# Performance work log

Measured on AMD Instinct MI355X. Metric: run time of the kernel, lower is better.

Reference implementation:

```python
import jax, jax.numpy as jnp
import numpy as np

N = 100000
E = 800000
D_IN = 64
D_HID = 64
D_OUT = 47


def gcn_conv(x, edge_index, W, b):
    # GCNConv with normalize=False: linear transform then sum-aggregate over edges.
    h = x @ W                              # [N, d_out]
    src, dst = edge_index[0], edge_index[1]
    msg = h[src]                           # [E, d_out] gather
    agg = jax.ops.segment_sum(msg, dst, num_segments=N)  # [N, d_out] scatter-add
    return agg + b


def setup_inputs() -> dict:
    key = jax.random.key(0)
    ks = jax.random.split(key, 8)
    x = jax.random.normal(ks[0], (N, D_IN), dtype=jnp.float32)
    edge_index = jax.random.randint(ks[1], (2, E), 0, N, dtype=jnp.int64)
    # Glorot-ish init for weights, zeros for bias (as in GCNConv.reset_parameters)
    def glorot(k, fan_in, fan_out):
        s = jnp.sqrt(6.0 / (fan_in + fan_out))
        return jax.random.uniform(k, (fan_in, fan_out), jnp.float32, -s, s)
    W1 = glorot(ks[2], D_IN, D_HID)
    b1 = jnp.zeros((D_HID,), jnp.float32)
    W2 = glorot(ks[3], D_HID, D_HID)
    b2 = jnp.zeros((D_HID,), jnp.float32)
    W3 = glorot(ks[4], D_HID, D_OUT)
    b3 = jnp.zeros((D_OUT,), jnp.float32)
    return {"x": x, "edge_index": edge_index,
            "W1": W1, "b1": b1, "W2": W2, "b2": b2, "W3": W3, "b3": b3}


def reference(x, edge_index, W1, b1, W2, b2, W3, b3):
    # Layer 1: conv -> relu (dropout is identity at inference)
    h = jax.nn.relu(gcn_conv(x, edge_index, W1, b1))
    # Layer 2
    h = jax.nn.relu(gcn_conv(h, edge_index, W2, b2))
    # Output layer + log_softmax over classes
    out = gcn_conv(h, edge_index, W3, b3)
    return jax.nn.log_softmax(out, axis=-1)
```

## Files before the change

kernel.cpp:

```cpp
#include <hip/hip_runtime.h>
#include <cmath>


#define B1_EPB 4096
#define BKT_SH 8
#define CHUNK  256
#define PSTRIDE 512

typedef __attribute__((ext_vector_type(8))) short bf8;
typedef __attribute__((ext_vector_type(4))) float f4;

__device__ __forceinline__ unsigned int f2bf(float x) {
  unsigned int u = __float_as_uint(x);
  return (u + 0x7FFFu + ((u >> 16) & 1u)) >> 16;
}
__device__ __forceinline__ float bflo(unsigned int u) { return __uint_as_float(u << 16); }
__device__ __forceinline__ float bfhi(unsigned int u) { return __uint_as_float(u & 0xFFFF0000u); }

__global__ void bhist_cvt_k(const int* __restrict__ dsti, int* __restrict__ part,
                            int ne, const float* __restrict__ x,
                            unsigned short* __restrict__ xb, int n4,
                            int nbkt, int nseg) {
  __shared__ int lh[PSTRIDE];
  const int b = blockIdx.x, t = threadIdx.x;
  if (b < nseg) {
    for (int i = t; i < PSTRIDE; i += 256) lh[i] = 0;
    __syncthreads();
    const int base = b * B1_EPB;
    const int m = min(B1_EPB, ne - base);
    for (int i = t; i < m; i += 256) atomicAdd(&lh[dsti[base + i] >> BKT_SH], 1);
    __syncthreads();
    for (int i = t; i < PSTRIDE; i += 256) part[b * PSTRIDE + i] = lh[i];
  }
  const int gid = b * 256 + t, gst = gridDim.x * 256;
  for (int j = gid; j < n4; j += gst) {
    float4 v = ((const float4*)x)[j];
    ushort4 o;
    o.x = (unsigned short)f2bf(v.x); o.y = (unsigned short)f2bf(v.y);
    o.z = (unsigned short)f2bf(v.z); o.w = (unsigned short)f2bf(v.w);
    ((ushort4*)xb)[j] = o;
  }
}

__global__ void btot_k(const int* __restrict__ part, int* __restrict__ btot,
                       int nseg) {
  __shared__ int sh[256];
  const int t = threadIdx.x;
  const int bkt = (blockIdx.x << 6) + (t & 63);
  int s0 = 0, s1 = 0, s2 = 0, s3 = 0, s4 = 0, s5 = 0, s6 = 0, s7 = 0;
  int seg = t >> 6;
  for (; seg + 28 < nseg; seg += 32) {
    s0 += part[(seg +  0) * PSTRIDE + bkt];
    s1 += part[(seg +  4) * PSTRIDE + bkt];
    s2 += part[(seg +  8) * PSTRIDE + bkt];
    s3 += part[(seg + 12) * PSTRIDE + bkt];
    s4 += part[(seg + 16) * PSTRIDE + bkt];
    s5 += part[(seg + 20) * PSTRIDE + bkt];
    s6 += part[(seg + 24) * PSTRIDE + bkt];
    s7 += part[(seg + 28) * PSTRIDE + bkt];
  }
  for (; seg < nseg; seg += 4) s0 += part[seg * PSTRIDE + bkt];
  sh[t] = ((s0 + s1) + (s2 + s3)) + ((s4 + s5) + (s6 + s7));
  __syncthreads();
  if (t < 64) btot[bkt] = sh[t] + sh[t + 64] + sh[t + 128] + sh[t + 192];
}

__global__ void bscan_k(const int* __restrict__ btot, int* __restrict__ bbase,
                        int* __restrict__ bcur, int nbkt, int ne) {
  __shared__ int sh[512];
  const int t = threadIdx.x;
  const int s = btot[t];
  sh[t] = s; __syncthreads();
  for (int o = 1; o < 512; o <<= 1) {
    int v = (t >= o) ? sh[t - o] : 0; __syncthreads();
    sh[t] += v; __syncthreads();
  }
  if (t < nbkt) { int e = sh[t] - s; bbase[t] = e; bcur[t] = e; }
  if (t == 0) bbase[nbkt] = ne;
}

__global__ void bucket_k(const int* __restrict__ srci, const int* __restrict__ dsti,
                         const int* __restrict__ part, int* __restrict__ bcur,
                         uint2* __restrict__ ebuf, int ne, int nbkt) {
  __shared__ int lcur[512], lbase[512];
  const int t = threadIdx.x;
  const int base = blockIdx.x * B1_EPB;
  const int m = min(B1_EPB, ne - base);
  for (int i = t; i < nbkt; i += 256) {
    const int c = part[blockIdx.x * PSTRIDE + i];
    lbase[i] = c ? atomicAdd(&bcur[i], c) : 0;
    lcur[i] = 0;
  }
  __syncthreads();
  for (int i = t; i < m; i += 256) {
    const int s = srci[base + i], d = dsti[base + i];
    const int b = d >> BKT_SH;
    const int p = lbase[b] + atomicAdd(&lcur[b], 1);
    ebuf[p] = make_uint2((unsigned)s, (unsigned)d);
  }
}

__global__ void fillb_k(const uint2* __restrict__ ebuf, const int* __restrict__ bbase,
                        int* __restrict__ row_off, int* __restrict__ ssrc,
                        int n, int ne) {
  __shared__ int lcnt[256], lpre[256], lcur[256];
  const int b = blockIdx.x, t = threadIdx.x;
  const int v0 = b << BKT_SH;
  const int nv = min(1 << BKT_SH, n - v0);
  const int start = bbase[b], end = bbase[b + 1];
  lcnt[t] = 0; __syncthreads();
  for (int i = start + t; i < end; i += 256)
    atomicAdd(&lcnt[ebuf[i].y & ((1 << BKT_SH) - 1)], 1);
  __syncthreads();
  const int x = lcnt[t];
  lpre[t] = x; __syncthreads();
  for (int o = 1; o < 256; o <<= 1) {
    int v = (t >= o) ? lpre[t - o] : 0; __syncthreads();
    lpre[t] += v; __syncthreads();
  }
  const int excl = start + lpre[t] - x;
  lcur[t] = excl;
  if (t < nv) row_off[v0 + t] = excl;
  if (t == 0) row_off[v0 + nv] = end;
  __syncthreads();
  for (int i = start + t; i < end; i += 256) {
    const uint2 e = ebuf[i];
    const int p = atomicAdd(&lcur[e.y & ((1 << BKT_SH) - 1)], 1);
    ssrc[p] = (int)e.x;
  }
}

template <int DOUT, bool LS>
__launch_bounds__(256, 4)
__global__ void fused_k(const unsigned short* __restrict__ in,
                        const int* __restrict__ row_off, const int* __restrict__ ssrc,
                        const float* __restrict__ Wm, const float* __restrict__ bin,
                        void* __restrict__ outp, int n) {
  constexpr int NT = (DOUT + 15) / 16;
  const int lane  = threadIdx.x & 63;
  const int wslot = threadIdx.x >> 6;
  const int quad  = lane >> 4;
  const int f16i  = lane & 15;

  __shared__ char rows_raw[4][16 * 144];
  __shared__ int  sidx[4][CHUNK];
  __shared__ unsigned short Wt[64 * 72];
  char* my  = rows_raw[wslot];
  int*  sid = sidx[wslot];

  {
    const int t = threadIdx.x;
    for (int i = t; i < 64 * 72; i += 256) Wt[i] = 0;
    __syncthreads();
    for (int i = t; i < 64 * DOUT; i += 256) {
      const int k = i / DOUT, c = i - k * DOUT;
      Wt[c * 72 + k] = (unsigned short)f2bf(Wm[i]);
    }
  }
  float bc[NT];
#pragma unroll
  for (int t = 0; t < NT; ++t) {
    const int c = t * 16 + f16i;
    bc[t] = (c < DOUT) ? bin[c] : 0.f;
  }
  __syncthreads();

  const uint2* in2 = (const uint2*)in;
  const int wid = (int)((blockIdx.x * blockDim.x + threadIdx.x) >> 6);
  const int nwv = (int)((gridDim.x * blockDim.x) >> 6);
  const int ntiles = (n + 15) >> 4;

  for (int tile = wid; tile < ntiles; tile += nwv) {
    const int v0 = tile << 4;
    const int ro_l = row_off[min(v0 + min(lane, 16), n)];
    const int base     = __shfl(ro_l, 0, 64);
    const int tile_end = __shfl(ro_l, 16, 64);
    int ns[4], nE[4];
#pragma unroll
    for (int r = 0; r < 4; ++r) {
      const int m = quad * 4 + r;
      ns[r] = __shfl(ro_l, m, 64);
      nE[r] = __shfl(ro_l, m + 1, 64);
    }

    float4 accA[4], accB[4];
#pragma unroll
    for (int r = 0; r < 4; ++r) {
      accA[r] = make_float4(0.f, 0.f, 0.f, 0.f);
      accB[r] = make_float4(0.f, 0.f, 0.f, 0.f);
    }

    for (int off = base; off < tile_end; off += CHUNK) {
      const int cend = min(tile_end, off + CHUNK);
      const int nL = cend - off;
#pragma unroll
      for (int k = 0; k < CHUNK / 64; ++k) {
        const int p = off + lane + k * 64;
        if (p < cend) sid[lane + k * 64] = ssrc[p];
      }
      asm volatile("s_waitcnt lgkmcnt(0)" ::: "memory");

#pragma unroll
      for (int r = 0; r < 4; ++r) {
        const int ls = max(ns[r], off), le = min(nE[r], cend);
        for (int c = ls; c < le; c += 8) {
          uint2 q[8];
#pragma unroll
          for (int k = 0; k < 8; ++k) {
            const int lofs = min(c - off + k, nL - 1);
            const int s = sid[lofs];
            q[k] = (c + k < le) ? in2[(size_t)s * 16 + f16i]
                                : make_uint2(0u, 0u);
          }
#pragma unroll
          for (int k = 0; k < 8; k += 2) {
            accA[r].x += bflo(q[k].x); accB[r].x += bflo(q[k + 1].x);
            accA[r].y += bfhi(q[k].x); accB[r].y += bfhi(q[k + 1].x);
            accA[r].z += bflo(q[k].y); accB[r].z += bflo(q[k + 1].y);
            accA[r].w += bfhi(q[k].y); accB[r].w += bfhi(q[k + 1].y);
          }
        }
      }
    }

#pragma unroll
    for (int r = 0; r < 4; ++r) {
      const int m = quad * 4 + r;
      uint2 p;
      p.x = f2bf(accA[r].x + accB[r].x) | (f2bf(accA[r].y + accB[r].y) << 16);
      p.y = f2bf(accA[r].z + accB[r].z) | (f2bf(accA[r].w + accB[r].w) << 16);
      *(uint2*)(my + m * 144 + f16i * 8) = p;
    }
    asm volatile("s_waitcnt lgkmcnt(0)" ::: "memory");

    bf8 a0 = *(const bf8*)(my + f16i * 144 + quad * 16);
    bf8 a1 = *(const bf8*)(my + f16i * 144 + quad * 16 + 64);
    f4 acc[NT];
#pragma unroll
    for (int t = 0; t < NT; ++t) {
      const unsigned short* wp = Wt + (t * 16 + f16i) * 72 + quad * 8;
      bf8 w0 = *(const bf8*)(wp);
      bf8 w1 = *(const bf8*)(wp + 32);
      f4 z = {0.f, 0.f, 0.f, 0.f};
      acc[t] = __builtin_amdgcn_mfma_f32_16x16x32_bf16(a0, w0, z, 0, 0, 0);
      acc[t] = __builtin_amdgcn_mfma_f32_16x16x32_bf16(a1, w1, acc[t], 0, 0, 0);
    }

    if (!LS) {
      unsigned short* ob = (unsigned short*)outp;
#pragma unroll
      for (int t = 0; t < NT; ++t)
#pragma unroll
        for (int j = 0; j < 4; ++j) {
          const int v = v0 + quad * 4 + j;
          if (v < n) {
            float val = acc[t][j] + bc[t];
            ob[(size_t)v * 64 + t * 16 + f16i] =
                (unsigned short)f2bf(fmaxf(val, 0.f));
          }
        }
    } else {
      float* ob = (float*)outp;
      float val[NT][4];
#pragma unroll
      for (int t = 0; t < NT; ++t)
#pragma unroll
        for (int j = 0; j < 4; ++j) val[t][j] = acc[t][j] + bc[t];
#pragma unroll
      for (int j = 0; j < 4; ++j) {
        float mx = -INFINITY;
#pragma unroll
        for (int t = 0; t < NT; ++t)
          if (t * 16 + f16i < DOUT) mx = fmaxf(mx, val[t][j]);
#pragma unroll
        for (int o = 1; o <= 8; o <<= 1) mx = fmaxf(mx, __shfl_xor(mx, o, 64));
        float sm = 0.f;
#pragma unroll
        for (int t = 0; t < NT; ++t)
          if (t * 16 + f16i < DOUT) sm += __expf(val[t][j] - mx);
#pragma unroll
        for (int o = 1; o <= 8; o <<= 1) sm += __shfl_xor(sm, o, 64);
        const float lse = mx + __logf(sm);
        const int v = v0 + quad * 4 + j;
        if (v < n) {
#pragma unroll
          for (int t = 0; t < NT; ++t) {
            const int c = t * 16 + f16i;
            if (c < DOUT) ob[(size_t)v * DOUT + c] = val[t][j] - lse;
          }
        }
      }
    }
  }
}

extern "C" void kernel_launch(void* const* d_in, const int* in_sizes, int n_in,
                              void* d_out, int out_size, void* d_ws, size_t ws_size,
                              hipStream_t stream) {
  const float* x  = (const float*)d_in[0];
  const int*   ei = (const int*)d_in[1];
  const float* W1 = (const float*)d_in[2];
  const float* b1 = (const float*)d_in[3];
  const float* W2 = (const float*)d_in[4];
  const float* b2 = (const float*)d_in[5];
  const float* W3 = (const float*)d_in[6];
  const float* b3 = (const float*)d_in[7];
  float* outp = (float*)d_out;

  const int n  = in_sizes[0] / 64;
  const int ne = in_sizes[1] / 2;
  const int* srci = ei;
  const int* dsti = ei + ne;
  const int nbkt = (n + (1 << BKT_SH) - 1) >> BKT_SH;
  const int nseg = (ne + B1_EPB - 1) / B1_EPB;

  const size_t N64 = (size_t)n * 64;
  unsigned short* xb   = (unsigned short*)d_ws;
  unsigned short* bufA = xb + N64;
  unsigned short* bufB = bufA + N64;
  uint2* ebuf   = (uint2*)(bufB + N64);
  int* row_off  = (int*)(ebuf + ne);
  int* part     = row_off + n + 1;
  int* bbase    = part + nseg * PSTRIDE;
  int* bcur     = bbase + nbkt + 1;
  int* btot     = bcur + nbkt;
  int* ssrc     = btot + 512;

  const int TB = 256;
  const int fus_blocks = 1568;

  bhist_cvt_k<<<784, TB, 0, stream>>>(dsti, part, ne, x, xb, (int)(N64 / 4), nbkt, nseg);
  btot_k<<<8, TB, 0, stream>>>(part, btot, nseg);
  bscan_k<<<1, 512, 0, stream>>>(btot, bbase, bcur, nbkt, ne);
  bucket_k<<<nseg, TB, 0, stream>>>(srci, dsti, part, bcur, ebuf, ne, nbkt);
  fillb_k<<<nbkt, TB, 0, stream>>>(ebuf, bbase, row_off, ssrc, n, ne);

  fused_k<64, false><<<fus_blocks, TB, 0, stream>>>(xb,   row_off, ssrc, W1, b1, bufA, n);
  fused_k<64, false><<<fus_blocks, TB, 0, stream>>>(bufA, row_off, ssrc, W2, b2, bufB, n);
  fused_k<47, true ><<<fus_blocks, TB, 0, stream>>>(bufB, row_off, ssrc, W3, b3, outp, n);
}
```

Before: 208.3 us.

## Fuse three GCN layer kernels into one persistent kernel with grid barriers

Replaces the three per-layer kernel launches with a single persistent kernel of 1024 blocks that runs all three layers, separated by a software grid barrier built on an atomic counter and spin-wait. Tiles are handed out through an atomic work-stealing counter per layer instead of a static grid-stride loop, which evens out load across waves on the skewed-degree graph. The goal is to cut launch gaps and tail imbalance. The barrier assumes all 1024 blocks are resident at once (four per CU at this register and LDS budget) and has a guard timeout that could silently break ordering if that assumption fails.

```diff
diff --git a/kernel.cpp b/kernel.cpp
--- a/kernel.cpp
+++ b/kernel.cpp
@@ -6,6 +6,7 @@
 #define BKT_SH 8
 #define CHUNK  256
 #define PSTRIDE 512
+#define FUS_BLOCKS 1024
 
 typedef __attribute__((ext_vector_type(8))) short bf8;
 typedef __attribute__((ext_vector_type(4))) float f4;
@@ -66,7 +67,9 @@
 }
 
 __global__ void bscan_k(const int* __restrict__ btot, int* __restrict__ bbase,
-                        int* __restrict__ bcur, int nbkt, int ne) {
+                        int* __restrict__ bcur, int nbkt, int ne,
+                        int* __restrict__ bar, int* __restrict__ steal,
+                        int nwaves) {
   __shared__ int sh[512];
   const int t = threadIdx.x;
   const int s = btot[t];
@@ -76,7 +79,11 @@
     sh[t] += v; __syncthreads();
   }
   if (t < nbkt) { int e = sh[t] - s; bbase[t] = e; bcur[t] = e; }
-  if (t == 0) bbase[nbkt] = ne;
+  if (t == 0) {
+    bbase[nbkt] = ne;
+    bar[0] = 0;
+    steal[0] = nwaves; steal[1] = nwaves; steal[2] = nwaves;
+  }
 }
 
 __global__ void bucket_k(const int* __restrict__ srci, const int* __restrict__ dsti,
@@ -130,32 +137,39 @@
   }
 }
 
+__device__ __forceinline__ void gridbar(int* bar, int target) {
+  __syncthreads();
+  if (threadIdx.x == 0) {
+    __hip_atomic_fetch_add(bar, 1, __ATOMIC_ACQ_REL, __HIP_MEMORY_SCOPE_AGENT);
+    int guard = 0;
+    while (__hip_atomic_load(bar, __ATOMIC_ACQUIRE, __HIP_MEMORY_SCOPE_AGENT) < target &&
+           guard < (1 << 22)) {
+      __builtin_amdgcn_s_sleep(8);
+      ++guard;
+    }
+  }
+  __syncthreads();
+}
+
 template <int DOUT, bool LS>
-__launch_bounds__(256, 4)
-__global__ void fused_k(const unsigned short* __restrict__ in,
-                        const int* __restrict__ row_off, const int* __restrict__ ssrc,
-                        const float* __restrict__ Wm, const float* __restrict__ bin,
-                        void* __restrict__ outp, int n) {
+__device__ __forceinline__ void layer_pass(
+    const unsigned short* __restrict__ in, const int* __restrict__ row_off,
+    const int* __restrict__ ssrc, const float* __restrict__ Wm,
+    const float* __restrict__ bin, void* __restrict__ outp, int n,
+    unsigned short* Wt, char* my, int* sid, int* steal, int wid) {
   constexpr int NT = (DOUT + 15) / 16;
-  const int lane  = threadIdx.x & 63;
-  const int wslot = threadIdx.x >> 6;
-  const int quad  = lane >> 4;
-  const int f16i  = lane & 15;
-
-  __shared__ char rows_raw[4][16 * 144];
-  __shared__ int  sidx[4][CHUNK];
-  __shared__ unsigned short Wt[64 * 72];
-  char* my  = rows_raw[wslot];
-  int*  sid = sidx[wslot];
-
-  {
-    const int t = threadIdx.x;
-    for (int i = t; i < 64 * 72; i += 256) Wt[i] = 0;
+  const int tid  = threadIdx.x;
+  const int lane = tid & 63;
+  const int quad = lane >> 4;
+  const int f16i = lane & 15;
+
+  if (DOUT < 64) {
+    for (int i = tid; i < 64 * 72; i += 256) Wt[i] = 0;
     __syncthreads();
-    for (int i = t; i < 64 * DOUT; i += 256) {
-      const int k = i / DOUT, c = i - k * DOUT;
-      Wt[c * 72 + k] = (unsigned short)f2bf(Wm[i]);
-    }
+  }
+  for (int i = tid; i < 64 * DOUT; i += 256) {
+    const int k = i / DOUT, c = i - k * DOUT;
+    Wt[c * 72 + k] = (unsigned short)f2bf(Wm[i]);
   }
   float bc[NT];
 #pragma unroll
@@ -166,11 +180,10 @@
   __syncthreads();
 
   const uint2* in2 = (const uint2*)in;
-  const int wid = (int)((blockIdx.x * blockDim.x + threadIdx.x) >> 6);
-  const int nwv = (int)((gridDim.x * blockDim.x) >> 6);
   const int ntiles = (n + 15) >> 4;
 
-  for (int tile = wid; tile < ntiles; tile += nwv) {
+  int tile = wid;
+  while (tile < ntiles) {
     const int v0 = tile << 4;
     const int ro_l = row_off[min(v0 + min(lane, 16), n)];
     const int base     = __shfl(ro_l, 0, 64);
@@ -291,7 +304,37 @@
         }
       }
     }
-  }
+
+    int nt_ = 0;
+    if (lane == 0) nt_ = atomicAdd(steal, 1);
+    tile = __shfl(nt_, 0, 64);
+  }
+}
+
+__launch_bounds__(256, 4)
+__global__ void fused3_k(const unsigned short* __restrict__ xb,
+                         unsigned short* __restrict__ bufA,
+                         unsigned short* __restrict__ bufB,
+                         float* __restrict__ outp,
+                         const int* __restrict__ row_off,
+                         const int* __restrict__ ssrc,
+                         const float* __restrict__ W1, const float* __restrict__ b1,
+                         const float* __restrict__ W2, const float* __restrict__ b2,
+                         const float* __restrict__ W3, const float* __restrict__ b3,
+                         int n, int* __restrict__ bar, int* __restrict__ steal) {
+  __shared__ char rows_raw[4][16 * 144];
+  __shared__ int  sidx[4][CHUNK];
+  __shared__ unsigned short Wt[64 * 72];
+  const int wslot = threadIdx.x >> 6;
+  char* my  = rows_raw[wslot];
+  int*  sid = sidx[wslot];
+  const int wid = (int)((blockIdx.x * 256 + threadIdx.x) >> 6);
+
+  layer_pass<64, false>(xb,   row_off, ssrc, W1, b1, bufA, n, Wt, my, sid, steal + 0, wid);
+  gridbar(bar, (int)gridDim.x);
+  layer_pass<64, false>(bufA, row_off, ssrc, W2, b2, bufB, n, Wt, my, sid, steal + 1, wid);
+  gridbar(bar, 2 * (int)gridDim.x);
+  layer_pass<47, true >(bufB, row_off, ssrc, W3, b3, outp, n, Wt, my, sid, steal + 2, wid);
 }
 
 extern "C" void kernel_launch(void* const* d_in, const int* in_sizes, int n_in,
@@ -324,18 +367,19 @@
   int* bbase    = part + nseg * PSTRIDE;
   int* bcur     = bbase + nbkt + 1;
   int* btot     = bcur + nbkt;
-  int* ssrc     = btot + 512;
+  int* bar      = btot + 512;
+  int* steal    = bar + 1;
+  int* ssrc     = steal + 3;
 
   const int TB = 256;
-  const int fus_blocks = 1568;
+  const int nwaves = FUS_BLOCKS * (TB / 64);
 
   bhist_cvt_k<<<784, TB, 0, stream>>>(dsti, part, ne, x, xb, (int)(N64 / 4), nbkt, nseg);
   btot_k<<<8, TB, 0, stream>>>(part, btot, nseg);
-  bscan_k<<<1, 512, 0, stream>>>(btot, bbase, bcur, nbkt, ne);
+  bscan_k<<<1, 512, 0, stream>>>(btot, bbase, bcur, nbkt, ne, bar, steal, nwaves);
   bucket_k<<<nseg, TB, 0, stream>>>(srci, dsti, part, bcur, ebuf, ne, nbkt);
   fillb_k<<<nbkt, TB, 0, stream>>>(ebuf, bbase, row_off, ssrc, n, ne);
 
-  fused_k<64, false><<<fus_blocks, TB, 0, stream>>>(xb,   row_off, ssrc, W1, b1, bufA, n);
-  fused_k<64, false><<<fus_blocks, TB, 0, stream>>>(bufA, row_off, ssrc, W2, b2, bufB, n);
-  fused_k<47, true ><<<fus_blocks, TB, 0, stream>>>(bufB, row_off, ssrc, W3, b3, outp, n);
-}
+  fused3_k<<<FUS_BLOCKS, TB, 0, stream>>>(xb, bufA, bufB, outp, row_off, ssrc,
+                                          W1, b1, W2, b2, W3, b3, n, bar, steal);
+}
```

Result: slower. 807.5 us (+287.8%).
